# Performance work log

Measured on AMD Instinct MI355X. Metric: run time of the kernel, lower is better.

The kernel has to match this reference:

```python
import jax, jax.numpy as jnp
import numpy as np

D_IN = 768
D_OUT = 768
NUM_HEADS = 12
HEAD_DIM = D_OUT // NUM_HEADS


def setup_inputs() -> dict:
    key = jax.random.key(0)
    ks = jax.random.split(key, 9)
    s = 1.0 / np.sqrt(D_IN)
    x = jax.random.normal(ks[0], (8, 1024, D_IN), dtype=jnp.float32)
    Wq = jax.random.uniform(ks[1], (D_IN, D_OUT), jnp.float32, -s, s)
    Wk = jax.random.uniform(ks[2], (D_IN, D_OUT), jnp.float32, -s, s)
    Wv = jax.random.uniform(ks[3], (D_IN, D_OUT), jnp.float32, -s, s)
    Wo = jax.random.uniform(ks[4], (D_OUT, D_OUT), jnp.float32, -s, s)
    bq = jax.random.uniform(ks[5], (D_OUT,), jnp.float32, -s, s)
    bk = jax.random.uniform(ks[6], (D_OUT,), jnp.float32, -s, s)
    bv = jax.random.uniform(ks[7], (D_OUT,), jnp.float32, -s, s)
    bo = jax.random.uniform(ks[8], (D_OUT,), jnp.float32, -s, s)
    return {"x": x, "Wq": Wq, "bq": bq, "Wk": Wk, "bk": bk,
            "Wv": Wv, "bv": bv, "Wo": Wo, "bo": bo}


def reference(x, Wq, bq, Wk, bk, Wv, bv, Wo, bo):
    b, n, _ = x.shape
    # projections -> (b, heads, n, head_dim)
    def split_heads(t):
        return t.reshape(b, n, NUM_HEADS, HEAD_DIM).transpose(0, 2, 1, 3)
    q = split_heads(x @ Wq + bq)
    k = split_heads(x @ Wk + bk)
    v = split_heads(x @ Wv + bv)
    scale = 1.0 / jnp.sqrt(jnp.float32(HEAD_DIM)).astype(x.dtype)
    scores = jnp.einsum('bhqd,bhkd->bhqk', q, k) * scale
    attn = jax.nn.softmax(scores, axis=-1)  # dropout p=0.0 -> identity
    ctx = jnp.einsum('bhqk,bhkd->bhqd', attn, v)
    ctx = ctx.transpose(0, 2, 1, 3).reshape(b, n, D_OUT)
    return ctx @ Wo + bo
```

## Files before the change

### kernel.cpp

```cpp
#include <hip/hip_runtime.h>
#include <math.h>

#define D_MODEL 768
#define NHEAD  12
#define HDIM   64
#define SEQ    1024
#define BATCH  8
#define MTOT   (BATCH*SEQ)
#define QKV_LD 2304

typedef _Float16 f16;
typedef __attribute__((ext_vector_type(2))) __fp16 fp16x2;
typedef __attribute__((ext_vector_type(4))) _Float16 f16x4;
typedef __attribute__((ext_vector_type(8))) _Float16 f16x8;
typedef __attribute__((ext_vector_type(4))) float f32x4;
typedef __attribute__((ext_vector_type(16))) float f32x16;

union PFrag { unsigned u[4]; f16x8 v; };
union PackW { fp16x2 h; unsigned u; };

__device__ inline void gload_lds16(const void* g, void* l) {
    __builtin_amdgcn_global_load_lds(
        (const __attribute__((address_space(1))) void*)g,
        (__attribute__((address_space(3))) void*)l, 16, 0, 0);
}

__global__ __launch_bounds__(256) void cvt_f32_f16_fused(
    const float* __restrict__ in, f16* __restrict__ out, int n8,
    const float* __restrict__ bq, const float* __restrict__ bk,
    const float* __restrict__ bv, float* __restrict__ bqkv)
{
    const int i = blockIdx.x * 256 + threadIdx.x;
    if (i < n8) {
        const float4 a = *(const float4*)(in + (size_t)i * 8);
        const float4 b = *(const float4*)(in + (size_t)i * 8 + 4);
        f16x8 v;
        v[0] = (f16)a.x; v[1] = (f16)a.y; v[2] = (f16)a.z; v[3] = (f16)a.w;
        v[4] = (f16)b.x; v[5] = (f16)b.y; v[6] = (f16)b.z; v[7] = (f16)b.w;
        *(f16x8*)(out + (size_t)i * 8) = v;
    }
    if (i < QKV_LD)
        bqkv[i] = (i < 768) ? bq[i] : (i < 1536) ? bk[i - 768] : bv[i - 1536];
}

__global__ __launch_bounds__(256) void transpose_cvt_all(
    const float* __restrict__ Wq, const float* __restrict__ Wk,
    const float* __restrict__ Wv, const float* __restrict__ Wo,
    f16* __restrict__ Wqkv_t, f16* __restrict__ Wo_t)
{
    const int z = blockIdx.z;
    const float* src = (z == 0) ? Wq : (z == 1) ? Wk : (z == 2) ? Wv : Wo;
    f16* dst = (z < 3) ? (Wqkv_t + (size_t)z * 768 * 768) : Wo_t;

    __shared__ f16 tile[64][72];
    const int t  = threadIdx.x;
    const int k0 = blockIdx.y * 64;
    const int n0 = blockIdx.x * 64;
    {
        const int r  = t >> 4;
        const int c4 = (t & 15) * 4;
        #pragma unroll
        for (int u = 0; u < 4; ++u) {
            const int row = r + u * 16;
            const float4 a = *(const float4*)&src[(size_t)(k0 + row) * 768 + n0 + c4];
            tile[row][c4 + 0] = (f16)a.x;
            tile[row][c4 + 1] = (f16)a.y;
            tile[row][c4 + 2] = (f16)a.z;
            tile[row][c4 + 3] = (f16)a.w;
        }
    }
    __syncthreads();
    {
        const int rn = t >> 3;
        const int ck = (t & 7) * 8;
        #pragma unroll
        for (int u = 0; u < 2; ++u) {
            const int n = rn + u * 32;
            f16x8 v;
            #pragma unroll
            for (int q = 0; q < 8; ++q) v[q] = tile[ck + q][n];
            *(f16x8*)&dst[(size_t)(n0 + n) * 768 + k0 + ck] = v;
        }
    }
}

template<typename OUT_T>
__global__ __launch_bounds__(256) void gemm_f16_tn(
    const f16* __restrict__ A, const f16* __restrict__ Bt,
    const float* __restrict__ bias, OUT_T* __restrict__ C,
    int M, int N, int K, int nb)
{
    __shared__ f16 As[128 * 64];
    __shared__ f16 Bs[128 * 64];

    const int t    = threadIdx.x;
    const int l15  = (t & 63) & 15;
    const int lg   = (t & 63) >> 4;
    const int w    = t >> 6;
    const int wrow = (w >> 1) * 64;
    const int wcol = (w & 1) * 64;

    const int orig = blockIdx.x;
    const int cpx  = gridDim.x >> 3;
    const int nid  = (orig & 7) * cpx + (orig >> 3);
    const int row0 = (nid / nb) * 128;
    const int col0 = (nid % nb) * 128;

    int src_row[4], src_koff[4], lds_off[4];
    #pragma unroll
    for (int i = 0; i < 4; ++i) {
        const int c = t + 256 * i;
        const int r = c >> 3;
        src_row[i]  = r;
        src_koff[i] = ((((c & 7) - (r >> 1)) & 7)) * 8;
        lds_off[i]  = c * 16;
    }

    int a_off[4][2], b_off[4][2];
    #pragma unroll
    for (int i = 0; i < 4; ++i) {
        const int ra = wrow + i * 16 + l15;
        const int rb = wcol + i * 16 + l15;
        #pragma unroll
        for (int s = 0; s < 2; ++s) {
            a_off[i][s] = ra * 128 + (((s * 4 + lg + (ra >> 1)) & 7) * 16);
            b_off[i][s] = rb * 128 + (((s * 4 + lg + (rb >> 1)) & 7) * 16);
        }
    }

    f32x4 acc[4][4];
    #pragma unroll
    for (int i = 0; i < 4; ++i)
        #pragma unroll
        for (int j = 0; j < 4; ++j)
            acc[i][j] = (f32x4){0.f, 0.f, 0.f, 0.f};

    const f16* Abase = A  + (size_t)row0 * K;
    const f16* Bbase = Bt + (size_t)col0 * K;

    for (int k0 = 0; k0 < K; k0 += 64) {
        #pragma unroll
        for (int i = 0; i < 4; ++i) {
            gload_lds16(Abase + (size_t)src_row[i] * K + k0 + src_koff[i],
                        (char*)As + lds_off[i]);
            gload_lds16(Bbase + (size_t)src_row[i] * K + k0 + src_koff[i],
                        (char*)Bs + lds_off[i]);
        }
        __syncthreads();

        #pragma unroll
        for (int s = 0; s < 2; ++s) {
            f16x8 af[4], bf[4];
            #pragma unroll
            for (int i = 0; i < 4; ++i) {
                af[i] = *(const f16x8*)((const char*)As + a_off[i][s]);
                bf[i] = *(const f16x8*)((const char*)Bs + b_off[i][s]);
            }
            #pragma unroll
            for (int i = 0; i < 4; ++i)
                #pragma unroll
                for (int j = 0; j < 4; ++j)
                    acc[i][j] = __builtin_amdgcn_mfma_f32_16x16x32_f16(
                        af[i], bf[j], acc[i][j], 0, 0, 0);
        }
        __syncthreads();
    }

    #pragma unroll
    for (int j = 0; j < 4; ++j) {
        const int col = col0 + wcol + j * 16 + l15;
        const float bj = bias[col];
        #pragma unroll
        for (int i = 0; i < 4; ++i) {
            const int row = row0 + wrow + i * 16 + lg * 4;
            #pragma unroll
            for (int q = 0; q < 4; ++q)
                C[(size_t)(row + q) * N + col] = (OUT_T)(acc[i][j][q] + bj);
        }
    }
}

#define QMAP(r, hh) (((r) & 3) + 8 * ((r) >> 2) + 4 * (hh))

__global__ __launch_bounds__(256, 3) void attn_f16(
    const f16* __restrict__ QKV, f16* __restrict__ O)
{
    __shared__ f16 KsB[2][64 * 64];
    __shared__ f16 VtB[2][64 * 64];

    const int t   = threadIdx.x;
    const int w   = t >> 6;
    const int l   = t & 63;
    const int l31 = l & 31;
    const int h   = l >> 5;
    const int sl  = (l & 7) << 4;

    const int orig = blockIdx.x;
    const int s    = (orig & 7) * 96 + (orig >> 3);
    const int bh   = s >> 3;
    const int qb   = s & 7;
    const int b  = bh / NHEAD;
    const int hd = bh % NHEAD;
    const int q0 = qb * 128;

    const size_t rowbase = (size_t)b * SEQ;
    const int qcol = hd * HDIM;
    const int kcol = 768 + hd * HDIM;
    const int vcol = 1536 + hd * HDIM;

    const f16 hsc = (f16)(0.125f * 1.4426950408889634f);
    f16x8 qf[4];
    #pragma unroll
    for (int dc = 0; dc < 4; ++dc) {
        f16x8 v = *(const f16x8*)(QKV
            + (rowbase + q0 + w * 32 + l31) * QKV_LD
            + qcol + dc * 16 + h * 8);
        #pragma unroll
        for (int j = 0; j < 8; ++j) v[j] *= hsc;
        qf[dc] = v;
    }

    f32x16 ctx[2];
    #pragma unroll
    for (int dt = 0; dt < 2; ++dt)
        #pragma unroll
        for (int r = 0; r < 16; ++r) ctx[dt][r] = 0.f;
    float lsum = 0.f;

    const int cb  = w * 16;
    const int vk0 = (l & 15) * 4;
    const int vd0 = ((l >> 4) + 4 * w) * 4;
    const f16* kptr = QKV + (rowbase + l)   * QKV_LD + kcol + cb;
    const f16* vptr = QKV + (rowbase + vk0) * QKV_LD + vcol + vd0;
    const size_t step = (size_t)64 * QKV_LD;

    f16x8 kr0, kr1;
    f16x4 vr[4];
    kr0 = *(const f16x8*)(kptr);
    kr1 = *(const f16x8*)(kptr + 8);
    #pragma unroll
    for (int i = 0; i < 4; ++i)
        vr[i] = *(const f16x4*)(vptr + (size_t)i * QKV_LD);

    {
        char* Kd = (char*)KsB[0];
        char* Vd = (char*)VtB[0];
        *(f16x8*)(Kd + l * 128 + ((cb * 2)      ^ sl)) = kr0;
        *(f16x8*)(Kd + l * 128 + ((cb * 2 + 16) ^ sl)) = kr1;
        #pragma unroll
        for (int di = 0; di < 4; ++di) {
            f16x4 wt;
            #pragma unroll
            for (int i = 0; i < 4; ++i) wt[i] = vr[i][di];
            *(f16x4*)(Vd + (vd0 + di) * 128
                         + ((vk0 * 2) ^ (((vd0 + di) & 7) << 4))) = wt;
        }
    }
    kr0 = *(const f16x8*)(kptr + step);
    kr1 = *(const f16x8*)(kptr + step + 8);
    #pragma unroll
    for (int i = 0; i < 4; ++i)
        vr[i] = *(const f16x4*)(vptr + step + (size_t)i * QKV_LD);
    __syncthreads();

    for (int kt = 0; kt < SEQ / 64; ++kt) {
        const int p = kt & 1;
        const char* Kp = (const char*)KsB[p];
        const char* Vp = (const char*)VtB[p];

        f32x16 sacc[2];
        __builtin_amdgcn_s_setprio(1);
        #pragma unroll
        for (int kk = 0; kk < 2; ++kk) {
            f32x16 a;
            #pragma unroll
            for (int r = 0; r < 16; ++r) a[r] = 0.f;
            #pragma unroll
            for (int dc = 0; dc < 4; ++dc) {
                const f16x8 ka = *(const f16x8*)(Kp + (kk * 32 + l31) * 128
                                                    + ((dc * 32 + h * 16) ^ sl));
                a = __builtin_amdgcn_mfma_f32_32x32x16_f16(ka, qf[dc], a, 0, 0, 0);
            }
            sacc[kk] = a;
        }
        __builtin_amdgcn_s_setprio(0);

        {
            float ps0 = 0.f, ps1 = 0.f, ps2 = 0.f, ps3 = 0.f;
            #pragma unroll
            for (int kk = 0; kk < 2; ++kk)
                #pragma unroll
                for (int r = 0; r < 16; r += 4) {
                    const float e0 = exp2f(sacc[kk][r + 0]);
                    const float e1 = exp2f(sacc[kk][r + 1]);
                    const float e2 = exp2f(sacc[kk][r + 2]);
                    const float e3 = exp2f(sacc[kk][r + 3]);
                    sacc[kk][r + 0] = e0; ps0 += e0;
                    sacc[kk][r + 1] = e1; ps1 += e1;
                    sacc[kk][r + 2] = e2; ps2 += e2;
                    sacc[kk][r + 3] = e3; ps3 += e3;
                }
            lsum += (ps0 + ps1) + (ps2 + ps3);
        }

        unsigned paw[4][4];
        #pragma unroll
        for (int kk = 0; kk < 2; ++kk) {
            unsigned dw[8];
            #pragma unroll
            for (int i = 0; i < 8; ++i) {
                PackW u;
                u.h = __builtin_amdgcn_cvt_pkrtz(sacc[kk][2 * i], sacc[kk][2 * i + 1]);
                dw[i] = u.u;
            }
            const unsigned t0 = (unsigned)__shfl_xor((int)(h ? dw[0] : dw[2]), 32);
            const unsigned t1 = (unsigned)__shfl_xor((int)(h ? dw[1] : dw[3]), 32);
            const unsigned t2 = (unsigned)__shfl_xor((int)(h ? dw[4] : dw[6]), 32);
            const unsigned t3 = (unsigned)__shfl_xor((int)(h ? dw[5] : dw[7]), 32);
            paw[2 * kk][0]     = h ? t0    : dw[0];
            paw[2 * kk][1]     = h ? t1    : dw[1];
            paw[2 * kk][2]     = h ? dw[2] : t0;
            paw[2 * kk][3]     = h ? dw[3] : t1;
            paw[2 * kk + 1][0] = h ? t2    : dw[4];
            paw[2 * kk + 1][1] = h ? t3    : dw[5];
            paw[2 * kk + 1][2] = h ? dw[6] : t2;
            paw[2 * kk + 1][3] = h ? dw[7] : t3;
        }

        if (kt < SEQ / 64 - 1) {
            char* Kd = (char*)KsB[p ^ 1];
            char* Vd = (char*)VtB[p ^ 1];
            *(f16x8*)(Kd + l * 128 + ((cb * 2)      ^ sl)) = kr0;
            *(f16x8*)(Kd + l * 128 + ((cb * 2 + 16) ^ sl)) = kr1;
            #pragma unroll
            for (int di = 0; di < 4; ++di) {
                f16x4 wt;
                #pragma unroll
                for (int i = 0; i < 4; ++i) wt[i] = vr[i][di];
                *(f16x4*)(Vd + (vd0 + di) * 128
                             + ((vk0 * 2) ^ (((vd0 + di) & 7) << 4))) = wt;
            }
            if (kt < SEQ / 64 - 2) {
                const f16* kp = kptr + (size_t)(kt + 2) * step;
                const f16* vp = vptr + (size_t)(kt + 2) * step;
                kr0 = *(const f16x8*)(kp);
                kr1 = *(const f16x8*)(kp + 8);
                #pragma unroll
                for (int i = 0; i < 4; ++i)
                    vr[i] = *(const f16x4*)(vp + (size_t)i * QKV_LD);
            }
        }

        __builtin_amdgcn_s_setprio(1);
        #pragma unroll
        for (int c = 0; c < 4; ++c) {
            PFrag pf;
            pf.u[0] = paw[c][0]; pf.u[1] = paw[c][1];
            pf.u[2] = paw[c][2]; pf.u[3] = paw[c][3];
            #pragma unroll
            for (int dt = 0; dt < 2; ++dt) {
                const f16x8 vb = *(const f16x8*)(Vp + (dt * 32 + l31) * 128
                                                    + ((c * 32 + h * 16) ^ sl));
                ctx[dt] = __builtin_amdgcn_mfma_f32_32x32x16_f16(pf.v, vb, ctx[dt], 0, 0, 0);
            }
        }
        __builtin_amdgcn_s_setprio(0);

        __syncthreads();
    }

    {
        const float ltot = lsum + __shfl_xor(lsum, 32);
        const float inv  = 1.0f / ltot;
        #pragma unroll
        for (int r = 0; r < 16; ++r) {
            const float iv = __shfl(inv, QMAP(r, h));
            const size_t row = rowbase + q0 + w * 32 + QMAP(r, h);
            O[row * D_MODEL + qcol + l31]      = (f16)(ctx[0][r] * iv);
            O[row * D_MODEL + qcol + 32 + l31] = (f16)(ctx[1][r] * iv);
        }
    }
}

extern "C" void kernel_launch(void* const* d_in, const int* in_sizes, int n_in,
                              void* d_out, int out_size, void* d_ws, size_t ws_size,
                              hipStream_t stream) {
    const float* x  = (const float*)d_in[0];
    const float* Wq = (const float*)d_in[1];
    const float* bq = (const float*)d_in[2];
    const float* Wk = (const float*)d_in[3];
    const float* bk = (const float*)d_in[4];
    const float* Wv = (const float*)d_in[5];
    const float* bv = (const float*)d_in[6];
    const float* Wo = (const float*)d_in[7];
    const float* bo = (const float*)d_in[8];
    float* out = (float*)d_out;

    char* ws = (char*)d_ws;
    f16*   QKV     = (f16*)(ws);
    f16*   xh      = (f16*)(ws + 37748736);
    f16*   ctxh    = (f16*)(ws + 37748736 + 12582912);
    f16*   Wqkv_t  = (f16*)(ws + 37748736 + 2 * 12582912);
    f16*   Wo_t    = (f16*)(ws + 37748736 + 2 * 12582912 + 3538944);
    float* bqkv    = (float*)(ws + 37748736 + 2 * 12582912 + 3538944 + 1179648);

    hipLaunchKernelGGL(cvt_f32_f16_fused, dim3(MTOT * D_MODEL / 8 / 256), dim3(256), 0, stream,
                       x, xh, MTOT * D_MODEL / 8, bq, bk, bv, bqkv);
    hipLaunchKernelGGL(transpose_cvt_all, dim3(12, 12, 4), dim3(256), 0, stream,
                       Wq, Wk, Wv, Wo, Wqkv_t, Wo_t);

    hipLaunchKernelGGL((gemm_f16_tn<f16>), dim3((QKV_LD / 128) * (MTOT / 128)), dim3(256), 0, stream,
                       xh, Wqkv_t, bqkv, QKV, MTOT, QKV_LD, D_MODEL, QKV_LD / 128);

    hipLaunchKernelGGL(attn_f16, dim3((SEQ / 128) * BATCH * NHEAD), dim3(256), 0, stream,
                       QKV, ctxh);

    hipLaunchKernelGGL((gemm_f16_tn<float>), dim3((D_MODEL / 128) * (MTOT / 128)), dim3(256), 0, stream,
                       ctxh, Wo_t, bo, out, MTOT, D_MODEL, D_MODEL, D_MODEL / 128);
}
```

Baseline: 136.4 us.

## Write V transposed from QKV GEMM and stream K/V into LDS directly

The QKV projection epilogue now stores Q and K in a narrower row-major buffer and writes V already transposed per head (d-major, token-contiguous). The attention kernel then loads K and V tiles with direct global-to-LDS 16-byte loads, replacing register staging and the per-tile LDS transpose of V. This cuts VGPR pressure and LDS write work in the attention loop. In exchange, the GEMM epilogue does scattered 8-byte transposed stores for V, and the LDS swizzle now depends on the global address pattern matching what the reader expects.

```diff
diff --git a/kernel.cpp b/kernel.cpp
--- a/kernel.cpp
+++ b/kernel.cpp
@@ -7,7 +7,8 @@
 #define SEQ    1024
 #define BATCH  8
 #define MTOT   (BATCH*SEQ)
-#define QKV_LD 2304
+#define QKV_N  2304
+#define QK_LD  1536
 
 typedef _Float16 f16;
 typedef __attribute__((ext_vector_type(2))) __fp16 fp16x2;
@@ -39,7 +40,7 @@
         v[4] = (f16)b.x; v[5] = (f16)b.y; v[6] = (f16)b.z; v[7] = (f16)b.w;
         *(f16x8*)(out + (size_t)i * 8) = v;
     }
-    if (i < QKV_LD)
+    if (i < QKV_N)
         bqkv[i] = (i < 768) ? bq[i] : (i < 1536) ? bk[i - 768] : bv[i - 1536];
 }
 
@@ -84,11 +85,12 @@
     }
 }
 
-template<typename OUT_T>
+template<typename OUT_T, bool SPLITV>
 __global__ __launch_bounds__(256) void gemm_f16_tn(
     const f16* __restrict__ A, const f16* __restrict__ Bt,
     const float* __restrict__ bias, OUT_T* __restrict__ C,
-    int M, int N, int K, int nb)
+    f16* __restrict__ Vt,
+    int M, int N, int K, int nb, int ldc)
 {
     __shared__ f16 As[128 * 64];
     __shared__ f16 Bs[128 * 64];
@@ -170,12 +172,27 @@
     for (int j = 0; j < 4; ++j) {
         const int col = col0 + wcol + j * 16 + l15;
         const float bj = bias[col];
-        #pragma unroll
-        for (int i = 0; i < 4; ++i) {
-            const int row = row0 + wrow + i * 16 + lg * 4;
-            #pragma unroll
-            for (int q = 0; q < 4; ++q)
-                C[(size_t)(row + q) * N + col] = (OUT_T)(acc[i][j][q] + bj);
+        if (!SPLITV || col < 1536) {
+            #pragma unroll
+            for (int i = 0; i < 4; ++i) {
+                const int row = row0 + wrow + i * 16 + lg * 4;
+                #pragma unroll
+                for (int q = 0; q < 4; ++q)
+                    C[(size_t)(row + q) * ldc + col] = (OUT_T)(acc[i][j][q] + bj);
+            }
+        } else if (SPLITV) {
+            const int h2 = (col - 1536) >> 6;
+            const int d  = (col - 1536) & 63;
+            #pragma unroll
+            for (int i = 0; i < 4; ++i) {
+                const int row = row0 + wrow + i * 16 + lg * 4;
+                const int bb  = row >> 10;
+                const int tok = row & 1023;
+                f16x4 v4;
+                #pragma unroll
+                for (int q = 0; q < 4; ++q) v4[q] = (f16)(acc[i][j][q] + bj);
+                *(f16x4*)(Vt + (((size_t)(bb * NHEAD + h2)) * 64 + d) * SEQ + tok) = v4;
+            }
         }
     }
 }
@@ -183,7 +200,8 @@
 #define QMAP(r, hh) (((r) & 3) + 8 * ((r) >> 2) + 4 * (hh))
 
 __global__ __launch_bounds__(256, 3) void attn_f16(
-    const f16* __restrict__ QKV, f16* __restrict__ O)
+    const f16* __restrict__ QK, const f16* __restrict__ Vt,
+    f16* __restrict__ O)
 {
     __shared__ f16 KsB[2][64 * 64];
     __shared__ f16 VtB[2][64 * 64];
@@ -205,15 +223,13 @@
 
     const size_t rowbase = (size_t)b * SEQ;
     const int qcol = hd * HDIM;
-    const int kcol = 768 + hd * HDIM;
-    const int vcol = 1536 + hd * HDIM;
 
     const f16 hsc = (f16)(0.125f * 1.4426950408889634f);
     f16x8 qf[4];
     #pragma unroll
     for (int dc = 0; dc < 4; ++dc) {
-        f16x8 v = *(const f16x8*)(QKV
-            + (rowbase + q0 + w * 32 + l31) * QKV_LD
+        f16x8 v = *(const f16x8*)(QK
+            + (rowbase + q0 + w * 32 + l31) * QK_LD
             + qcol + dc * 16 + h * 8);
         #pragma unroll
         for (int j = 0; j < 8; ++j) v[j] *= hsc;
@@ -227,44 +243,33 @@
         for (int r = 0; r < 16; ++r) ctx[dt][r] = 0.f;
     float lsum = 0.f;
 
-    const int cb  = w * 16;
-    const int vk0 = (l & 15) * 4;
-    const int vd0 = ((l >> 4) + 4 * w) * 4;
-    const f16* kptr = QKV + (rowbase + l)   * QKV_LD + kcol + cb;
-    const f16* vptr = QKV + (rowbase + vk0) * QKV_LD + vcol + vd0;
-    const size_t step = (size_t)64 * QKV_LD;
-
-    f16x8 kr0, kr1;
-    f16x4 vr[4];
-    kr0 = *(const f16x8*)(kptr);
-    kr1 = *(const f16x8*)(kptr + 8);
-    #pragma unroll
-    for (int i = 0; i < 4; ++i)
-        vr[i] = *(const f16x4*)(vptr + (size_t)i * QKV_LD);
-
-    {
-        char* Kd = (char*)KsB[0];
-        char* Vd = (char*)VtB[0];
-        *(f16x8*)(Kd + l * 128 + ((cb * 2)      ^ sl)) = kr0;
-        *(f16x8*)(Kd + l * 128 + ((cb * 2 + 16) ^ sl)) = kr1;
-        #pragma unroll
-        for (int di = 0; di < 4; ++di) {
-            f16x4 wt;
-            #pragma unroll
-            for (int i = 0; i < 4; ++i) wt[i] = vr[i][di];
-            *(f16x4*)(Vd + (vd0 + di) * 128
-                         + ((vk0 * 2) ^ (((vd0 + di) & 7) << 4))) = wt;
-        }
-    }
-    kr0 = *(const f16x8*)(kptr + step);
-    kr1 = *(const f16x8*)(kptr + step + 8);
-    #pragma unroll
-    for (int i = 0; i < 4; ++i)
-        vr[i] = *(const f16x4*)(vptr + step + (size_t)i * QKV_LD);
+    const int rsub   = l >> 3;
+    const int schunk = (l & 7) ^ rsub;
+    const f16* ksrc = QK + (rowbase + w * 16 + rsub) * QK_LD
+                         + 768 + qcol + schunk * 8;
+    const f16* vsrc = Vt + (((size_t)bh * 64) + w * 16 + rsub) * SEQ
+                         + schunk * 8;
+    const size_t kstep = (size_t)64 * QK_LD;
+    const int    woff  = w * 2048;
+
+    gload_lds16(ksrc,             (char*)KsB[0] + woff);
+    gload_lds16(ksrc + 8 * QK_LD, (char*)KsB[0] + woff + 1024);
+    gload_lds16(vsrc,             (char*)VtB[0] + woff);
+    gload_lds16(vsrc + 8 * SEQ,   (char*)VtB[0] + woff + 1024);
     __syncthreads();
 
     for (int kt = 0; kt < SEQ / 64; ++kt) {
         const int p = kt & 1;
+
+        if (kt < SEQ / 64 - 1) {
+            const f16* ks = ksrc + (size_t)(kt + 1) * kstep;
+            const f16* vs = vsrc + (kt + 1) * 64;
+            gload_lds16(ks,             (char*)KsB[p ^ 1] + woff);
+            gload_lds16(ks + 8 * QK_LD, (char*)KsB[p ^ 1] + woff + 1024);
+            gload_lds16(vs,             (char*)VtB[p ^ 1] + woff);
+            gload_lds16(vs + 8 * SEQ,   (char*)VtB[p ^ 1] + woff + 1024);
+        }
+
         const char* Kp = (const char*)KsB[p];
         const char* Vp = (const char*)VtB[p];
 
@@ -327,30 +332,6 @@
             paw[2 * kk + 1][3] = h ? dw[7] : t3;
         }
 
-        if (kt < SEQ / 64 - 1) {
-            char* Kd = (char*)KsB[p ^ 1];
-            char* Vd = (char*)VtB[p ^ 1];
-            *(f16x8*)(Kd + l * 128 + ((cb * 2)      ^ sl)) = kr0;
-            *(f16x8*)(Kd + l * 128 + ((cb * 2 + 16) ^ sl)) = kr1;
-            #pragma unroll
-            for (int di = 0; di < 4; ++di) {
-                f16x4 wt;
-                #pragma unroll
-                for (int i = 0; i < 4; ++i) wt[i] = vr[i][di];
-                *(f16x4*)(Vd + (vd0 + di) * 128
-                             + ((vk0 * 2) ^ (((vd0 + di) & 7) << 4))) = wt;
-            }
-            if (kt < SEQ / 64 - 2) {
-                const f16* kp = kptr + (size_t)(kt + 2) * step;
-                const f16* vp = vptr + (size_t)(kt + 2) * step;
-                kr0 = *(const f16x8*)(kp);
-                kr1 = *(const f16x8*)(kp + 8);
-                #pragma unroll
-                for (int i = 0; i < 4; ++i)
-                    vr[i] = *(const f16x4*)(vp + (size_t)i * QKV_LD);
-            }
-        }
-
         __builtin_amdgcn_s_setprio(1);
         #pragma unroll
         for (int c = 0; c < 4; ++c) {
@@ -397,24 +378,25 @@
     float* out = (float*)d_out;
 
     char* ws = (char*)d_ws;
-    f16*   QKV     = (f16*)(ws);
+    f16*   QKb     = (f16*)(ws);
+    f16*   Vt      = (f16*)(ws + 25165824);
     f16*   xh      = (f16*)(ws + 37748736);
-    f16*   ctxh    = (f16*)(ws + 37748736 + 12582912);
-    f16*   Wqkv_t  = (f16*)(ws + 37748736 + 2 * 12582912);
-    f16*   Wo_t    = (f16*)(ws + 37748736 + 2 * 12582912 + 3538944);
-    float* bqkv    = (float*)(ws + 37748736 + 2 * 12582912 + 3538944 + 1179648);
+    f16*   ctxh    = (f16*)(ws + 50331648);
+    f16*   Wqkv_t  = (f16*)(ws + 62914560);
+    f16*   Wo_t    = (f16*)(ws + 66453504);
+    float* bqkv    = (float*)(ws + 67633152);
 
     hipLaunchKernelGGL(cvt_f32_f16_fused, dim3(MTOT * D_MODEL / 8 / 256), dim3(256), 0, stream,
                        x, xh, MTOT * D_MODEL / 8, bq, bk, bv, bqkv);
     hipLaunchKernelGGL(transpose_cvt_all, dim3(12, 12, 4), dim3(256), 0, stream,
                        Wq, Wk, Wv, Wo, Wqkv_t, Wo_t);
 
-    hipLaunchKernelGGL((gemm_f16_tn<f16>), dim3((QKV_LD / 128) * (MTOT / 128)), dim3(256), 0, stream,
-                       xh, Wqkv_t, bqkv, QKV, MTOT, QKV_LD, D_MODEL, QKV_LD / 128);
+    hipLaunchKernelGGL((gemm_f16_tn<f16, true>), dim3((QKV_N / 128) * (MTOT / 128)), dim3(256), 0, stream,
+                       xh, Wqkv_t, bqkv, QKb, Vt, MTOT, QKV_N, D_MODEL, QKV_N / 128, QK_LD);
 
     hipLaunchKernelGGL(attn_f16, dim3((SEQ / 128) * BATCH * NHEAD), dim3(256), 0, stream,
-                       QKV, ctxh);
-
-    hipLaunchKernelGGL((gemm_f16_tn<float>), dim3((D_MODEL / 128) * (MTOT / 128)), dim3(256), 0, stream,
-                       ctxh, Wo_t, bo, out, MTOT, D_MODEL, D_MODEL, D_MODEL / 128);
-}
+                       QKb, Vt, ctxh);
+
+    hipLaunchKernelGGL((gemm_f16_tn<float, false>), dim3((D_MODEL / 128) * (MTOT / 128)), dim3(256), 0, stream,
+                       ctxh, Wo_t, bo, out, (f16*)nullptr, MTOT, D_MODEL, D_MODEL, D_MODEL / 128, D_MODEL);
+}
```

After: 123.4 us. 9.5% less time.
